# Optimization experiments

Hardware: AMD Instinct MI355X
Metric: run time of the kernel (lower is better)

The kernel has to match this reference:

```python
import jax, jax.numpy as jnp
import numpy as np

HEAD_NUM = 16
NEG_BIG = 1e12


def setup_inputs() -> dict:
    key = jax.random.key(0)
    ks = jax.random.split(key, 10)
    B, S, H = 4, 2048, 1024
    std = 0.02
    return {
        "encoder_outputs": jax.random.normal(ks[0], (B, S, H), dtype=jnp.float32),
        "mask": jax.random.randint(ks[1], (B, S), 0, 2, dtype=jnp.int32),
        "Wq": jax.random.normal(ks[2], (H, H), dtype=jnp.float32) * std,
        "bq": jax.random.normal(ks[3], (H,), dtype=jnp.float32) * std,
        "Wk": jax.random.normal(ks[4], (H, H), dtype=jnp.float32) * std,
        "bk": jax.random.normal(ks[5], (H,), dtype=jnp.float32) * std,
        "Wv": jax.random.normal(ks[6], (H, H), dtype=jnp.float32) * std,
        "bv": jax.random.normal(ks[7], (H,), dtype=jnp.float32) * std,
        "Wc": jax.random.normal(ks[8], (H, H), dtype=jnp.float32) * std,
    }


def _split_heads(x, h):
    # chunk(h, -1) + stack(dim=0): [B,S,H] -> [h,B,S,H//h]
    B, S, H = x.shape
    return jnp.moveaxis(x.reshape(B, S, h, H // h), 2, 0)


def reference(encoder_outputs, mask, Wq, bq, Wk, bk, Wv, bv, Wc):
    x = encoder_outputs
    B, S, H = x.shape
    hd = H // HEAD_NUM
    q = _split_heads(x @ Wq.T + bq, HEAD_NUM)  # [h,B,S,hd]
    k = _split_heads(x @ Wk.T + bk, HEAD_NUM)
    v = _split_heads(x @ Wv.T + bv, HEAD_NUM)
    dots = jnp.einsum("hbqd,hbkd->hbqk", q, k) / jnp.sqrt(jnp.float32(hd))
    m = mask.astype(jnp.float32)  # [B,S]; 0 = valid token
    inv = 1.0 - m
    eye = jnp.eye(S, dtype=jnp.float32)
    # clamp_max(1 - (1-m)_i (1-m)_j + eye, 1): [B,S,S]
    new_mask = jnp.minimum(1.0 - inv[:, :, None] * inv[:, None, :] + eye, 1.0)
    energies = dots - new_mask[None] * NEG_BIG
    weights = jax.nn.softmax(energies, axis=-1) * (1.0 - new_mask)[None]
    out = jnp.einsum("hbqk,hbkd->hbqd", weights, v)  # [h,B,S,hd]
    out = jnp.moveaxis(out, 0, 2).reshape(B, S, H)  # concat heads
    return out @ Wc.T
```

## Files before the change

### kernel.cpp

```cpp
#include <hip/hip_runtime.h>
#include <cstddef>
#include <cstdint>

#define BB 4
#define SS 2048
#define HH 1024
#define NH 16
#define HD 64

typedef _Float16 half8 __attribute__((ext_vector_type(8)));
typedef _Float16 half4v __attribute__((ext_vector_type(4)));
typedef float f32x4 __attribute__((ext_vector_type(4)));

#define KSCALE 0.1803368801111f

__device__ __forceinline__ void gload_lds16(const _Float16* g, char* l) {
    __builtin_amdgcn_global_load_lds(
        (const __attribute__((address_space(1))) void*)g,
        (__attribute__((address_space(3))) void*)l, 16, 0, 0);
}

__global__ __launch_bounds__(256)
void scan_mask(const int* __restrict__ mk, int* __restrict__ vidx,
               int* __restrict__ ividx, int* __restrict__ cnt)
{
    __shared__ int ps[256];
    const int b = blockIdx.x, t = threadIdx.x;
    int flag[8], s = 0;
#pragma unroll
    for (int k = 0; k < 8; ++k) { flag[k] = (mk[(b << 11) + t * 8 + k] == 0); s += flag[k]; }
    ps[t] = s;
    __syncthreads();
    for (int off = 1; off < 256; off <<= 1) {
        const int add = (t >= off) ? ps[t - off] : 0;
        __syncthreads();
        ps[t] += add;
        __syncthreads();
    }
    int posv = ps[t] - s;
#pragma unroll
    for (int k = 0; k < 8; ++k) {
        const int gidx = t * 8 + k;
        if (flag[k]) vidx[(b << 11) + posv++] = gidx;
        else         ividx[(b << 11) + (gidx - posv)] = gidx;
    }
    if (t == 255) cnt[b] = ps[255];
}

__global__ __launch_bounds__(256)
void prep_rows(const float* __restrict__ x, const int* __restrict__ vidx,
               const int* __restrict__ ividx, const int* __restrict__ cnt,
               _Float16* __restrict__ xc, float* __restrict__ out)
{
    const int row = blockIdx.x;
    const int b = row >> 11, i = row & 2047;
    const int t = threadIdx.x;
    const int cb = cnt[b];
    half4v hv = (half4v){0, 0, 0, 0};
    if (i < cb) {
        const float4 v = ((const float4*)(x + (size_t)((b << 11) + vidx[row]) * HH))[t];
        hv[0] = (_Float16)v.x; hv[1] = (_Float16)v.y;
        hv[2] = (_Float16)v.z; hv[3] = (_Float16)v.w;
    }
    ((half4v*)(xc + (size_t)row * HH))[t] = hv;
    if (i < SS - cb) {
        float* p = out + (size_t)((b << 11) + ividx[row]) * HH;
        ((float4*)p)[t] = make_float4(0.f, 0.f, 0.f, 0.f);
    }
}

__global__ __launch_bounds__(256)
void cvt_w(const float* __restrict__ Wq, const float* __restrict__ Wk,
           const float* __restrict__ Wv, const float* __restrict__ Wc,
           _Float16* __restrict__ o)
{
    const float* src = blockIdx.z == 0 ? Wq : blockIdx.z == 1 ? Wk :
                       blockIdx.z == 2 ? Wv : Wc;
    _Float16* dst = o + (size_t)blockIdx.z * (HH * HH);
    const int i = blockIdx.x * 256 + threadIdx.x;
    const float4 v0 = ((const float4*)src)[(size_t)i * 2];
    const float4 v1 = ((const float4*)src)[(size_t)i * 2 + 1];
    half8 hv;
    hv[0] = (_Float16)v0.x; hv[1] = (_Float16)v0.y;
    hv[2] = (_Float16)v0.z; hv[3] = (_Float16)v0.w;
    hv[4] = (_Float16)v1.x; hv[5] = (_Float16)v1.y;
    hv[6] = (_Float16)v1.z; hv[7] = (_Float16)v1.w;
    ((half8*)dst)[i] = hv;
}

__device__ __forceinline__ void gemm_core128(const _Float16* __restrict__ A,
                                             const _Float16* __restrict__ W,
                                             int K, int m0, int n0,
                                             char* As, char* Bs, f32x4 acc[4][4])
{
    const int t = threadIdx.x;
    const int w = t >> 6, lane = t & 63;
    const int ln = lane & 15, g = lane >> 4;
    const int wr = w >> 1, wc = w & 1;

    const int rr0 = w * 16 + (lane >> 2);
    const int rr1 = rr0 + 64;
    const int p   = lane & 3;
    const int sl0 = p ^ ((rr0 >> 1) & 3);
    const int sl1 = p ^ ((rr1 >> 1) & 3);
    const _Float16* ga0 = A + (size_t)(m0 + rr0) * K + sl0 * 8;
    const _Float16* ga1 = A + (size_t)(m0 + rr1) * K + sl1 * 8;
    const _Float16* gb0 = W + (size_t)(n0 + rr0) * K + sl0 * 8;
    const _Float16* gb1 = W + (size_t)(n0 + rr1) * K + sl1 * 8;
    char* dA = As + w * 1024 + lane * 16;
    char* dB = Bs + w * 1024 + lane * 16;

    int offA[4], offB[4];
#pragma unroll
    for (int i = 0; i < 4; ++i) {
        const int ra = wr * 64 + i * 16 + ln;
        offA[i] = ra * 64 + ((g ^ ((ra >> 1) & 3)) << 4);
        const int rb = wc * 64 + i * 16 + ln;
        offB[i] = rb * 64 + ((g ^ ((rb >> 1) & 3)) << 4);
    }

#pragma unroll
    for (int i = 0; i < 4; ++i)
#pragma unroll
        for (int j = 0; j < 4; ++j) acc[i][j] = (f32x4){0.f, 0.f, 0.f, 0.f};

    gload_lds16(ga0, dA);
    gload_lds16(ga1, dA + 4096);
    gload_lds16(gb0, dB);
    gload_lds16(gb1, dB + 4096);
    gload_lds16(ga0 + 32, dA + 8192);
    gload_lds16(ga1 + 32, dA + 8192 + 4096);
    gload_lds16(gb0 + 32, dB + 8192);
    gload_lds16(gb1 + 32, dB + 8192 + 4096);

    const int ns = K / 32;
    for (int k = 0; k < ns; ++k) {
        if (k < ns - 1) { asm volatile("s_waitcnt vmcnt(4)" ::: "memory"); }
        else            { asm volatile("s_waitcnt vmcnt(0)" ::: "memory"); }
        __builtin_amdgcn_s_barrier();
        __builtin_amdgcn_sched_barrier(0);

        const char* Ab = As + ((k & 1) << 13);
        const char* Bb = Bs + ((k & 1) << 13);
        half8 af[4], bf[4];
#pragma unroll
        for (int i = 0; i < 4; ++i) af[i] = *(const half8*)(Ab + offA[i]);
#pragma unroll
        for (int j = 0; j < 4; ++j) bf[j] = *(const half8*)(Bb + offB[j]);

        asm volatile("s_waitcnt lgkmcnt(0)" ::: "memory");
        __builtin_amdgcn_s_barrier();
        __builtin_amdgcn_sched_barrier(0);

        if (k + 2 < ns) {
            const int nb = (k & 1) << 13;
            const int ko = (k + 2) * 32;
            gload_lds16(ga0 + ko, dA + nb);
            gload_lds16(ga1 + ko, dA + nb + 4096);
            gload_lds16(gb0 + ko, dB + nb);
            gload_lds16(gb1 + ko, dB + nb + 4096);
        }
#pragma unroll
        for (int i = 0; i < 4; ++i)
#pragma unroll
            for (int j = 0; j < 4; ++j)
                acc[i][j] = __builtin_amdgcn_mfma_f32_16x16x32_f16(af[i], bf[j], acc[i][j], 0, 0, 0);
    }
}

__global__ __launch_bounds__(512, 2)
void gemm_qkv(const _Float16* __restrict__ xc, const _Float16* __restrict__ W16,
              const float* __restrict__ bq, const float* __restrict__ bk,
              const float* __restrict__ bv, const int* __restrict__ cnt,
              _Float16* __restrict__ Qh, _Float16* __restrict__ Kh,
              _Float16* __restrict__ Vt)
{
    const int yb = blockIdx.y;
    const int bI = yb & 3;
    const int mt = yb >> 2;
    if (mt * 256 >= ((cnt[bI] + 255) & ~255)) return;
    const int m0 = (bI << 11) + mt * 256;

    __shared__ __align__(16) char As[32768];
    __shared__ __align__(16) char Bs[32768];
    const int n0 = blockIdx.x * 256;
    const int z = n0 >> 10;
    const float* bias = (z == 0) ? bq : (z == 1) ? bk : bv;

    const int t = threadIdx.x;
    const int w = t >> 6, lane = t & 63;
    const int ln = lane & 15, g = lane >> 4;
    const int wr = w >> 2, wc = w & 3;

    const int rr0 = t >> 2;
    const int rr1 = rr0 + 128;
    const int p   = t & 3;
    const int sl0 = p ^ ((rr0 >> 1) & 3);
    const int sl1 = p ^ ((rr1 >> 1) & 3);
    const _Float16* ga0 = xc  + (size_t)(m0 + rr0) * HH + sl0 * 8;
    const _Float16* ga1 = xc  + (size_t)(m0 + rr1) * HH + sl1 * 8;
    const _Float16* gb0 = W16 + (size_t)(n0 + rr0) * HH + sl0 * 8;
    const _Float16* gb1 = W16 + (size_t)(n0 + rr1) * HH + sl1 * 8;
    char* dA = As + t * 16;
    char* dB = Bs + t * 16;

    int offA[8], offB[4];
#pragma unroll
    for (int i = 0; i < 8; ++i) {
        const int ra = wr * 128 + i * 16 + ln;
        offA[i] = ra * 64 + ((g ^ ((ra >> 1) & 3)) << 4);
    }
#pragma unroll
    for (int j = 0; j < 4; ++j) {
        const int rb = wc * 64 + j * 16 + ln;
        offB[j] = rb * 64 + ((g ^ ((rb >> 1) & 3)) << 4);
    }

    f32x4 acc[8][4];
#pragma unroll
    for (int i = 0; i < 8; ++i)
#pragma unroll
        for (int j = 0; j < 4; ++j) acc[i][j] = (f32x4){0.f, 0.f, 0.f, 0.f};

    gload_lds16(ga0, dA);
    gload_lds16(ga1, dA + 8192);
    gload_lds16(gb0, dB);
    gload_lds16(gb1, dB + 8192);
    gload_lds16(ga0 + 32, dA + 16384);
    gload_lds16(ga1 + 32, dA + 16384 + 8192);
    gload_lds16(gb0 + 32, dB + 16384);
    gload_lds16(gb1 + 32, dB + 16384 + 8192);

    const int ns = HH / 32;
    for (int k = 0; k < ns; ++k) {
        if (k < ns - 1) { asm volatile("s_waitcnt vmcnt(4)" ::: "memory"); }
        else            { asm volatile("s_waitcnt vmcnt(0)" ::: "memory"); }
        __builtin_amdgcn_s_barrier();
        __builtin_amdgcn_sched_barrier(0);

        const char* Ab = As + ((k & 1) << 14);
        const char* Bb = Bs + ((k & 1) << 14);
        half8 af[8], bf[4];
#pragma unroll
        for (int i = 0; i < 8; ++i) af[i] = *(const half8*)(Ab + offA[i]);
#pragma unroll
        for (int j = 0; j < 4; ++j) bf[j] = *(const half8*)(Bb + offB[j]);

        asm volatile("s_waitcnt lgkmcnt(0)" ::: "memory");
        __builtin_amdgcn_s_barrier();
        __builtin_amdgcn_sched_barrier(0);

        if (k + 2 < ns) {
            const int nb = (k & 1) << 14;
            const int ko = (k + 2) * 32;
            gload_lds16(ga0 + ko, dA + nb);
            gload_lds16(ga1 + ko, dA + nb + 8192);
            gload_lds16(gb0 + ko, dB + nb);
            gload_lds16(gb1 + ko, dB + nb + 8192);
        }
#pragma unroll
        for (int i = 0; i < 8; ++i)
#pragma unroll
            for (int j = 0; j < 4; ++j)
                acc[i][j] = __builtin_amdgcn_mfma_f32_16x16x32_f16(af[i], bf[j], acc[i][j], 0, 0, 0);
    }

    const int mBase = m0 + wr * 128 + g * 4;
    const int nBase = n0 + wc * 64 + ln;
    if (z < 2) {
        _Float16* O = z ? Kh : Qh;
        const float sc = z ? 1.0f : KSCALE;
#pragma unroll
        for (int j = 0; j < 4; ++j) {
            const int nn = (nBase + j * 16) & 1023;
            const int h = nn >> 6, d = nn & 63;
            const float bvf = bias[nn];
#pragma unroll
            for (int i = 0; i < 8; ++i) {
                const int m = mBase + i * 16;
                const int b = m >> 11, s = m & 2047;
                _Float16* dst = O + (((size_t)(b * NH + h) * SS + s) * HD + d);
#pragma unroll
                for (int r = 0; r < 4; ++r)
                    dst[(size_t)r * HD] = (_Float16)((acc[i][j][r] + bvf) * sc);
            }
        }
    } else {
#pragma unroll
        for (int j = 0; j < 4; ++j) {
            const int nn = (nBase + j * 16) & 1023;
            const int h = nn >> 6, d = nn & 63;
            const float bvf = bias[nn];
#pragma unroll
            for (int i = 0; i < 8; ++i) {
                const int m = mBase + i * 16;
                const int b = m >> 11, s = m & 2047;
                const int sp = (s & ~31) | (((s >> 2) & 3) << 3) | (((s >> 4) & 1) << 2);
                half4v v;
#pragma unroll
                for (int r = 0; r < 4; ++r) v[r] = (_Float16)(acc[i][j][r] + bvf);
                *(half4v*)(Vt + ((size_t)(b * NH + h) * HD + d) * SS + sp) = v;
            }
        }
    }
}

__global__ __launch_bounds__(256)
void gemm_out(const _Float16* __restrict__ Oc, const _Float16* __restrict__ Wc16,
              const int* __restrict__ cnt, const int* __restrict__ vidx,
              float* __restrict__ C)
{
    const int yb = blockIdx.y;
    const int bI = yb & 3;
    const int mt = yb >> 2;
    const int cb = cnt[bI];
    if (mt * 128 >= ((cb + 127) & ~127)) return;
    const int m0 = (bI << 11) + mt * 128;

    __shared__ __align__(16) char As[16384];
    __shared__ __align__(16) char Bs[16384];
    const int n0 = blockIdx.x * 128;

    f32x4 acc[4][4];
    gemm_core128(Oc, Wc16, HH, m0, n0, As, Bs, acc);

    const int t = threadIdx.x;
    const int w = t >> 6, lane = t & 63;
    const int ln = lane & 15, g = lane >> 4;
    const int wr = w >> 1, wc = w & 1;
    const int mBase = m0 + wr * 64 + g * 4;
    const int nBase = n0 + wc * 64 + ln;
#pragma unroll
    for (int i = 0; i < 4; ++i) {
#pragma unroll
        for (int r = 0; r < 4; ++r) {
            const int m = mBase + i * 16 + r;
            const int lm = m & 2047;
            if (lm < cb) {
                const int orig = vidx[m];
                const size_t off = (size_t)((m & ~2047) + orig) * HH + nBase;
#pragma unroll
                for (int j = 0; j < 4; ++j)
                    C[off + j * 16] = acc[i][j][r];
            }
        }
    }
}

__global__ __launch_bounds__(512, 4)
void attn_mfma(const _Float16* __restrict__ Qh, const _Float16* __restrict__ Kh,
               const _Float16* __restrict__ Vt, const int* __restrict__ cnt,
               _Float16* __restrict__ Oc)
{
    __shared__ __align__(16) char ksm[3][8192];
    __shared__ __align__(16) char vsm[3][8192];

    const int t  = threadIdx.x;
    const int w  = t >> 6, l = t & 63, ln = l & 15, g = l >> 4;
    const int bh = blockIdx.x;
    const int b  = bh >> 4, h = bh & 15;
    const int cb = cnt[b];
    const int q0 = blockIdx.y << 6;
    if (q0 >= cb) return;
    const int p  = w & 3;
    const int hf = w >> 2;
    const int qw = q0 + (p << 4);
    const bool active = (qw < cb);
    const int nt = (cb + 63) >> 6;
    const int jtd = qw >> 6;
    const int rel = (qw & 63) + ln;

    half8 qf[2];
    f32x4 oacc[4];
    float lrun = 0.f;
    if (active) {
        const int qg = qw + ln;
        const _Float16* qp = Qh + ((size_t)bh * SS + qg) * HD + g * 8;
        qf[0] = *(const half8*)qp;
        qf[1] = *(const half8*)(qp + 32);
#pragma unroll
        for (int dd = 0; dd < 4; ++dd) oacc[dd] = (f32x4){0.f, 0.f, 0.f, 0.f};
    }

    const int sr = t >> 3;
    const int sl = (t & 7) ^ (sr & 7);
    const _Float16* kbase = Kh + ((size_t)bh * SS + sr) * HD + sl * 8;
    const _Float16* vbase = Vt + ((size_t)bh * HD + sr) * SS + sl * 8;

    gload_lds16(kbase, ksm[0] + t * 16);
    gload_lds16(vbase, vsm[0] + t * 16);
    if (nt > 1) {
        gload_lds16(kbase + (size_t)64 * HD, ksm[1] + t * 16);
        gload_lds16(vbase + 64,              vsm[1] + t * 16);
    }

    int cur = 0;
    for (int jt = 0; jt < nt; ++jt) {
        if (jt < nt - 1) { asm volatile("s_waitcnt vmcnt(2) lgkmcnt(0)" ::: "memory"); }
        else             { asm volatile("s_waitcnt vmcnt(0) lgkmcnt(0)" ::: "memory"); }
        __builtin_amdgcn_s_barrier();
        __builtin_amdgcn_sched_barrier(0);

        if (jt + 2 < nt) {
            const int nb = (cur + 2 >= 3) ? cur - 1 : cur + 2;
            const int jn = (jt + 2) << 6;
            gload_lds16(kbase + (size_t)jn * HD, ksm[nb] + t * 16);
            gload_lds16(vbase + jn,              vsm[nb] + t * 16);
        }

        if (active) {
            const int j0 = jt << 6;
            const char* kb = ksm[cur];
            const char* vb = vsm[cur];
            half8 kf[2][2];
#pragma unroll
            for (int tu = 0; tu < 2; ++tu) {
                const int row = (hf * 2 + tu) * 16 + ln;
                const int sw  = (row & 7) << 4;
                const int rb  = row * 128;
                kf[tu][0] = *(const half8*)(kb + ((rb + g * 16)      ^ sw));
                kf[tu][1] = *(const half8*)(kb + ((rb + 64 + g * 16) ^ sw));
            }
            const bool slow = (jt == jtd) | (j0 + 64 > cb);

            f32x4 sa[2];
            __builtin_amdgcn_s_setprio(1);
#pragma unroll
            for (int tu = 0; tu < 2; ++tu) {
                sa[tu] = (f32x4){0.f, 0.f, 0.f, 0.f};
                sa[tu] = __builtin_amdgcn_mfma_f32_16x16x32_f16(kf[tu][0], qf[0], sa[tu], 0, 0, 0);
                sa[tu] = __builtin_amdgcn_mfma_f32_16x16x32_f16(kf[tu][1], qf[1], sa[tu], 0, 0, 0);
            }
            __builtin_amdgcn_s_setprio(0);

            float wv[2][4];
#pragma unroll
            for (int tu = 0; tu < 2; ++tu)
#pragma unroll
                for (int r = 0; r < 4; ++r) {
                    float tv = sa[tu][r];
                    if (slow) {
                        const int kp = (hf * 2 + tu) * 16 + g * 4 + r;
                        if (((jt == jtd) & (kp == rel)) | (j0 + kp >= cb))
                            tv = -1e30f;
                    }
                    wv[tu][r] = exp2f(tv);
                }
            lrun += ((wv[0][0] + wv[0][1]) + (wv[0][2] + wv[0][3]))
                  + ((wv[1][0] + wv[1][1]) + (wv[1][2] + wv[1][3]));

            half8 pf;
            pf[0] = (_Float16)wv[0][0]; pf[1] = (_Float16)wv[0][1];
            pf[2] = (_Float16)wv[0][2]; pf[3] = (_Float16)wv[0][3];
            pf[4] = (_Float16)wv[1][0]; pf[5] = (_Float16)wv[1][1];
            pf[6] = (_Float16)wv[1][2]; pf[7] = (_Float16)wv[1][3];

            __builtin_amdgcn_s_setprio(1);
#pragma unroll
            for (int dd = 0; dd < 4; ++dd) {
                const int row = dd * 16 + ln;
                const int sw  = (row & 7) << 4;
                const int rb  = row * 128;
                const half8 vf = *(const half8*)(vb + ((rb + hf * 64 + g * 16) ^ sw));
                oacc[dd] = __builtin_amdgcn_mfma_f32_16x16x32_f16(vf, pf, oacc[dd], 0, 0, 0);
            }
            __builtin_amdgcn_s_setprio(0);
        }
        cur = (cur + 1 == 3) ? 0 : cur + 1;
    }

    __syncthreads();
    f32x4* cmo = (f32x4*)vsm;
    float* cml = (float*)(cmo + 1024);
    if (active && hf == 1) {
#pragma unroll
        for (int dd = 0; dd < 4; ++dd) cmo[(p * 4 + dd) * 64 + l] = oacc[dd];
        cml[p * 64 + l] = lrun;
    }
    __syncthreads();
    if (active && hf == 0) {
#pragma unroll
        for (int dd = 0; dd < 4; ++dd) oacc[dd] += cmo[(p * 4 + dd) * 64 + l];
        float ls = lrun + cml[p * 64 + l];
        ls += __shfl_xor(ls, 16);
        ls += __shfl_xor(ls, 32);
        const int iq = qw + ln;
        if (iq < cb) {
            const float inv = (ls > 0.f) ? 1.f / ls : 0.f;
            _Float16* op = Oc + ((size_t)((b << 11) + iq)) * HH + h * HD + g * 4;
#pragma unroll
            for (int dd = 0; dd < 4; ++dd) {
                half4v hv;
#pragma unroll
                for (int r = 0; r < 4; ++r) hv[r] = (_Float16)(oacc[dd][r] * inv);
                *(half4v*)(op + dd * 16) = hv;
            }
        }
    }
}

extern "C" void kernel_launch(void* const* d_in, const int* in_sizes, int n_in,
                              void* d_out, int out_size, void* d_ws, size_t ws_size,
                              hipStream_t stream)
{
    (void)in_sizes; (void)n_in; (void)out_size; (void)ws_size;

    const float* x  = (const float*)d_in[0];
    const int*   mk = (const int*)d_in[1];
    const float* Wq = (const float*)d_in[2];
    const float* bq = (const float*)d_in[3];
    const float* Wk = (const float*)d_in[4];
    const float* bk = (const float*)d_in[5];
    const float* Wv = (const float*)d_in[6];
    const float* bv = (const float*)d_in[7];
    const float* Wc = (const float*)d_in[8];
    float* out = (float*)d_out;

    const int M = BB * SS;
    const size_t NE = (size_t)M * HH;
    const size_t NW = (size_t)HH * HH;
    _Float16* xc  = (_Float16*)d_ws;
    _Float16* W16 = xc + NE;
    _Float16* Qh  = W16 + 4 * NW;
    _Float16* Kh  = Qh + NE;
    _Float16* Vt  = Kh + NE;
    _Float16* Oc  = Vt + NE;
    int* vidx  = (int*)(Oc + NE);
    int* cnt   = vidx + M;
    int* ividx = cnt + 64;

    scan_mask<<<BB, 256, 0, stream>>>(mk, vidx, ividx, cnt);
    prep_rows<<<M, 256, 0, stream>>>(x, vidx, ividx, cnt, xc, out);
    cvt_w<<<dim3(512, 1, 4), 256, 0, stream>>>(Wq, Wk, Wv, Wc, W16);

    dim3 gq(3 * HH / 256, M / 256);
    gemm_qkv<<<gq, 512, 0, stream>>>(xc, W16, bq, bk, bv, cnt, Qh, Kh, Vt);

    dim3 ga(BB * NH, SS / 64);
    attn_mfma<<<ga, 512, 0, stream>>>(Qh, Kh, Vt, cnt, Oc);

    dim3 go(HH / 128, M / 128);
    gemm_out<<<go, 256, 0, stream>>>(Oc, W16 + 3 * NW, cnt, vidx, out);
}
```

Measured before the change: 122.9 us.

## Process two query sub-tiles per wave in attention to reuse K/V fragments

Each attention block now covers 128 query rows instead of 64. Each wave handles two 16-row query slices, so every K and V fragment read from LDS feeds two MFMAs, and each K/V tile loaded into shared memory serves twice as many queries. This halves the number of blocks and the total K/V traffic into shared memory. The cost is more registers (launch bounds lowered from 4 to 2 blocks per CU), fewer blocks to spread across the CUs, and a cross-wave combine step that now loops twice with extra barriers.

```diff
diff --git a/kernel.cpp b/kernel.cpp
--- a/kernel.cpp
+++ b/kernel.cpp
@@ -347,7 +347,7 @@
     }
 }
 
-__global__ __launch_bounds__(512, 4)
+__global__ __launch_bounds__(512, 2)
 void attn_mfma(const _Float16* __restrict__ Qh, const _Float16* __restrict__ Kh,
                const _Float16* __restrict__ Vt, const int* __restrict__ cnt,
                _Float16* __restrict__ Oc)
@@ -360,26 +360,30 @@
     const int bh = blockIdx.x;
     const int b  = bh >> 4, h = bh & 15;
     const int cb = cnt[b];
-    const int q0 = blockIdx.y << 6;
+    const int q0 = blockIdx.y << 7;
     if (q0 >= cb) return;
     const int p  = w & 3;
     const int hf = w >> 2;
-    const int qw = q0 + (p << 4);
+    const int qw = q0 + (p << 5);
     const bool active = (qw < cb);
     const int nt = (cb + 63) >> 6;
     const int jtd = qw >> 6;
-    const int rel = (qw & 63) + ln;
-
-    half8 qf[2];
-    f32x4 oacc[4];
-    float lrun = 0.f;
+    const int relb = (qw & 63) + ln;
+
+    half8 qf[2][2];
+    f32x4 oacc[2][4];
+    float lrun[2];
     if (active) {
-        const int qg = qw + ln;
-        const _Float16* qp = Qh + ((size_t)bh * SS + qg) * HD + g * 8;
-        qf[0] = *(const half8*)qp;
-        qf[1] = *(const half8*)(qp + 32);
-#pragma unroll
-        for (int dd = 0; dd < 4; ++dd) oacc[dd] = (f32x4){0.f, 0.f, 0.f, 0.f};
+#pragma unroll
+        for (int qs = 0; qs < 2; ++qs) {
+            const int qg = qw + qs * 16 + ln;
+            const _Float16* qp = Qh + ((size_t)bh * SS + qg) * HD + g * 8;
+            qf[qs][0] = *(const half8*)qp;
+            qf[qs][1] = *(const half8*)(qp + 32);
+            lrun[qs] = 0.f;
+#pragma unroll
+            for (int dd = 0; dd < 4; ++dd) oacc[qs][dd] = (f32x4){0.f, 0.f, 0.f, 0.f};
+        }
     }
 
     const int sr = t >> 3;
@@ -423,37 +427,44 @@
             }
             const bool slow = (jt == jtd) | (j0 + 64 > cb);
 
-            f32x4 sa[2];
+            f32x4 sa[2][2];
             __builtin_amdgcn_s_setprio(1);
 #pragma unroll
             for (int tu = 0; tu < 2; ++tu) {
-                sa[tu] = (f32x4){0.f, 0.f, 0.f, 0.f};
-                sa[tu] = __builtin_amdgcn_mfma_f32_16x16x32_f16(kf[tu][0], qf[0], sa[tu], 0, 0, 0);
-                sa[tu] = __builtin_amdgcn_mfma_f32_16x16x32_f16(kf[tu][1], qf[1], sa[tu], 0, 0, 0);
+#pragma unroll
+                for (int qs = 0; qs < 2; ++qs) {
+                    sa[qs][tu] = (f32x4){0.f, 0.f, 0.f, 0.f};
+                    sa[qs][tu] = __builtin_amdgcn_mfma_f32_16x16x32_f16(kf[tu][0], qf[qs][0], sa[qs][tu], 0, 0, 0);
+                    sa[qs][tu] = __builtin_amdgcn_mfma_f32_16x16x32_f16(kf[tu][1], qf[qs][1], sa[qs][tu], 0, 0, 0);
+                }
             }
             __builtin_amdgcn_s_setprio(0);
 
-            float wv[2][4];
-#pragma unroll
-            for (int tu = 0; tu < 2; ++tu)
-#pragma unroll
-                for (int r = 0; r < 4; ++r) {
-                    float tv = sa[tu][r];
-                    if (slow) {
-                        const int kp = (hf * 2 + tu) * 16 + g * 4 + r;
-                        if (((jt == jtd) & (kp == rel)) | (j0 + kp >= cb))
-                            tv = -1e30f;
+            half8 pf[2];
+#pragma unroll
+            for (int qs = 0; qs < 2; ++qs) {
+                float wv[2][4];
+#pragma unroll
+                for (int tu = 0; tu < 2; ++tu)
+#pragma unroll
+                    for (int r = 0; r < 4; ++r) {
+                        float tv = sa[qs][tu][r];
+                        if (slow) {
+                            const int kp = (hf * 2 + tu) * 16 + g * 4 + r;
+                            if (((jt == jtd) & (kp == relb + qs * 16)) | (j0 + kp >= cb))
+                                tv = -1e30f;
+                        }
+                        wv[tu][r] = exp2f(tv);
                     }
-                    wv[tu][r] = exp2f(tv);
-                }
-            lrun += ((wv[0][0] + wv[0][1]) + (wv[0][2] + wv[0][3]))
-                  + ((wv[1][0] + wv[1][1]) + (wv[1][2] + wv[1][3]));
-
-            half8 pf;
-            pf[0] = (_Float16)wv[0][0]; pf[1] = (_Float16)wv[0][1];
-            pf[2] = (_Float16)wv[0][2]; pf[3] = (_Float16)wv[0][3];
-            pf[4] = (_Float16)wv[1][0]; pf[5] = (_Float16)wv[1][1];
-            pf[6] = (_Float16)wv[1][2]; pf[7] = (_Float16)wv[1][3];
+                lrun[qs] += ((wv[0][0] + wv[0][1]) + (wv[0][2] + wv[0][3]))
+                          + ((wv[1][0] + wv[1][1]) + (wv[1][2] + wv[1][3]));
+                half8 pp;
+                pp[0] = (_Float16)wv[0][0]; pp[1] = (_Float16)wv[0][1];
+                pp[2] = (_Float16)wv[0][2]; pp[3] = (_Float16)wv[0][3];
+                pp[4] = (_Float16)wv[1][0]; pp[5] = (_Float16)wv[1][1];
+                pp[6] = (_Float16)wv[1][2]; pp[7] = (_Float16)wv[1][3];
+                pf[qs] = pp;
+            }
 
             __builtin_amdgcn_s_setprio(1);
 #pragma unroll
@@ -462,38 +473,44 @@
                 const int sw  = (row & 7) << 4;
                 const int rb  = row * 128;
                 const half8 vf = *(const half8*)(vb + ((rb + hf * 64 + g * 16) ^ sw));
-                oacc[dd] = __builtin_amdgcn_mfma_f32_16x16x32_f16(vf, pf, oacc[dd], 0, 0, 0);
+#pragma unroll
+                for (int qs = 0; qs < 2; ++qs)
+                    oacc[qs][dd] = __builtin_amdgcn_mfma_f32_16x16x32_f16(vf, pf[qs], oacc[qs][dd], 0, 0, 0);
             }
             __builtin_amdgcn_s_setprio(0);
         }
         cur = (cur + 1 == 3) ? 0 : cur + 1;
     }
 
-    __syncthreads();
-    f32x4* cmo = (f32x4*)vsm;
-    float* cml = (float*)(cmo + 1024);
-    if (active && hf == 1) {
-#pragma unroll
-        for (int dd = 0; dd < 4; ++dd) cmo[(p * 4 + dd) * 64 + l] = oacc[dd];
-        cml[p * 64 + l] = lrun;
-    }
-    __syncthreads();
-    if (active && hf == 0) {
-#pragma unroll
-        for (int dd = 0; dd < 4; ++dd) oacc[dd] += cmo[(p * 4 + dd) * 64 + l];
-        float ls = lrun + cml[p * 64 + l];
-        ls += __shfl_xor(ls, 16);
-        ls += __shfl_xor(ls, 32);
-        const int iq = qw + ln;
-        if (iq < cb) {
-            const float inv = (ls > 0.f) ? 1.f / ls : 0.f;
-            _Float16* op = Oc + ((size_t)((b << 11) + iq)) * HH + h * HD + g * 4;
-#pragma unroll
-            for (int dd = 0; dd < 4; ++dd) {
-                half4v hv;
-#pragma unroll
-                for (int r = 0; r < 4; ++r) hv[r] = (_Float16)(oacc[dd][r] * inv);
-                *(half4v*)(op + dd * 16) = hv;
+    f32x4* cmo = (f32x4*)ksm;
+    float*  cml = (float*)vsm;
+#pragma unroll
+    for (int qs = 0; qs < 2; ++qs) {
+        __syncthreads();
+        if (active && hf == 1) {
+#pragma unroll
+            for (int dd = 0; dd < 4; ++dd) cmo[(p * 4 + dd) * 64 + l] = oacc[qs][dd];
+            cml[p * 64 + l] = lrun[qs];
+        }
+        __syncthreads();
+        if (active && hf == 0) {
+            f32x4 o[4];
+#pragma unroll
+            for (int dd = 0; dd < 4; ++dd) o[dd] = oacc[qs][dd] + cmo[(p * 4 + dd) * 64 + l];
+            float ls = lrun[qs] + cml[p * 64 + l];
+            ls += __shfl_xor(ls, 16);
+            ls += __shfl_xor(ls, 32);
+            const int iq = qw + qs * 16 + ln;
+            if (iq < cb) {
+                const float inv = (ls > 0.f) ? 1.f / ls : 0.f;
+                _Float16* op = Oc + ((size_t)((b << 11) + iq)) * HH + h * HD + g * 4;
+#pragma unroll
+                for (int dd = 0; dd < 4; ++dd) {
+                    half4v hv;
+#pragma unroll
+                    for (int r = 0; r < 4; ++r) hv[r] = (_Float16)(o[dd][r] * inv);
+                    *(half4v*)(op + dd * 16) = hv;
+                }
             }
         }
     }
@@ -536,7 +553,7 @@
     dim3 gq(3 * HH / 256, M / 256);
     gemm_qkv<<<gq, 512, 0, stream>>>(xc, W16, bq, bk, bv, cnt, Qh, Kh, Vt);
 
-    dim3 ga(BB * NH, SS / 64);
+    dim3 ga(BB * NH, SS / 128);
     attn_mfma<<<ga, 512, 0, stream>>>(Qh, Kh, Vt, cnt, Oc);
 
     dim3 go(HH / 128, M / 128);
```

Result: slower. 134.0 us (+9.1%).

## Merge weight conversion into prep kernel and double-buffer attention K/V

Applied to the files above, without the earlier changes.

Folds the fp32-to-fp16 weight conversion into the row-prep kernel as extra blocks, removing one kernel launch and letting both run concurrently. In the attention kernel, the three-stage K/V LDS ring becomes a two-stage double buffer, cutting shared memory from 48KB to 32KB, which may allow more resident blocks. The cost is less prefetch depth: each iteration now waits for every outstanding load before computing. The combine scratch is moved to fit within the smaller buffers.

```diff
diff --git a/kernel.cpp b/kernel.cpp
--- a/kernel.cpp
+++ b/kernel.cpp
@@ -50,11 +50,30 @@
 __global__ __launch_bounds__(256)
 void prep_rows(const float* __restrict__ x, const int* __restrict__ vidx,
                const int* __restrict__ ividx, const int* __restrict__ cnt,
-               _Float16* __restrict__ xc, float* __restrict__ out)
-{
-    const int row = blockIdx.x;
+               _Float16* __restrict__ xc, float* __restrict__ out,
+               const float* __restrict__ Wq, const float* __restrict__ Wk,
+               const float* __restrict__ Wv, const float* __restrict__ Wc,
+               _Float16* __restrict__ W16)
+{
+    const int t = threadIdx.x;
+    const int blk = blockIdx.x;
+    if (blk >= BB * SS) {
+        const int wi = (blk - BB * SS) * 256 + t;
+        const int z = wi >> 17, idx = wi & 131071;
+        const float* src = z == 0 ? Wq : z == 1 ? Wk : z == 2 ? Wv : Wc;
+        _Float16* dst = W16 + (size_t)z * (HH * HH);
+        const float4 v0 = ((const float4*)src)[(size_t)idx * 2];
+        const float4 v1 = ((const float4*)src)[(size_t)idx * 2 + 1];
+        half8 hv;
+        hv[0] = (_Float16)v0.x; hv[1] = (_Float16)v0.y;
+        hv[2] = (_Float16)v0.z; hv[3] = (_Float16)v0.w;
+        hv[4] = (_Float16)v1.x; hv[5] = (_Float16)v1.y;
+        hv[6] = (_Float16)v1.z; hv[7] = (_Float16)v1.w;
+        ((half8*)dst)[idx] = hv;
+        return;
+    }
+    const int row = blk;
     const int b = row >> 11, i = row & 2047;
-    const int t = threadIdx.x;
     const int cb = cnt[b];
     half4v hv = (half4v){0, 0, 0, 0};
     if (i < cb) {
@@ -67,25 +86,6 @@
         float* p = out + (size_t)((b << 11) + ividx[row]) * HH;
         ((float4*)p)[t] = make_float4(0.f, 0.f, 0.f, 0.f);
     }
-}
-
-__global__ __launch_bounds__(256)
-void cvt_w(const float* __restrict__ Wq, const float* __restrict__ Wk,
-           const float* __restrict__ Wv, const float* __restrict__ Wc,
-           _Float16* __restrict__ o)
-{
-    const float* src = blockIdx.z == 0 ? Wq : blockIdx.z == 1 ? Wk :
-                       blockIdx.z == 2 ? Wv : Wc;
-    _Float16* dst = o + (size_t)blockIdx.z * (HH * HH);
-    const int i = blockIdx.x * 256 + threadIdx.x;
-    const float4 v0 = ((const float4*)src)[(size_t)i * 2];
-    const float4 v1 = ((const float4*)src)[(size_t)i * 2 + 1];
-    half8 hv;
-    hv[0] = (_Float16)v0.x; hv[1] = (_Float16)v0.y;
-    hv[2] = (_Float16)v0.z; hv[3] = (_Float16)v0.w;
-    hv[4] = (_Float16)v1.x; hv[5] = (_Float16)v1.y;
-    hv[6] = (_Float16)v1.z; hv[7] = (_Float16)v1.w;
-    ((half8*)dst)[i] = hv;
 }
 
 __device__ __forceinline__ void gemm_core128(const _Float16* __restrict__ A,
@@ -352,8 +352,8 @@
                const _Float16* __restrict__ Vt, const int* __restrict__ cnt,
                _Float16* __restrict__ Oc)
 {
-    __shared__ __align__(16) char ksm[3][8192];
-    __shared__ __align__(16) char vsm[3][8192];
+    __shared__ __align__(16) char ksm[2][8192];
+    __shared__ __align__(16) char vsm[2][8192];
 
     const int t  = threadIdx.x;
     const int w  = t >> 6, l = t & 63, ln = l & 15, g = l >> 4;
@@ -389,23 +389,17 @@
 
     gload_lds16(kbase, ksm[0] + t * 16);
     gload_lds16(vbase, vsm[0] + t * 16);
-    if (nt > 1) {
-        gload_lds16(kbase + (size_t)64 * HD, ksm[1] + t * 16);
-        gload_lds16(vbase + 64,              vsm[1] + t * 16);
-    }
 
     int cur = 0;
     for (int jt = 0; jt < nt; ++jt) {
-        if (jt < nt - 1) { asm volatile("s_waitcnt vmcnt(2) lgkmcnt(0)" ::: "memory"); }
-        else             { asm volatile("s_waitcnt vmcnt(0) lgkmcnt(0)" ::: "memory"); }
+        asm volatile("s_waitcnt vmcnt(0) lgkmcnt(0)" ::: "memory");
         __builtin_amdgcn_s_barrier();
         __builtin_amdgcn_sched_barrier(0);
 
-        if (jt + 2 < nt) {
-            const int nb = (cur + 2 >= 3) ? cur - 1 : cur + 2;
-            const int jn = (jt + 2) << 6;
-            gload_lds16(kbase + (size_t)jn * HD, ksm[nb] + t * 16);
-            gload_lds16(vbase + jn,              vsm[nb] + t * 16);
+        if (jt + 1 < nt) {
+            const int jn = (jt + 1) << 6;
+            gload_lds16(kbase + (size_t)jn * HD, ksm[cur ^ 1] + t * 16);
+            gload_lds16(vbase + jn,              vsm[cur ^ 1] + t * 16);
         }
 
         if (active) {
@@ -466,12 +460,12 @@
             }
             __builtin_amdgcn_s_setprio(0);
         }
-        cur = (cur + 1 == 3) ? 0 : cur + 1;
+        cur ^= 1;
     }
 
     __syncthreads();
-    f32x4* cmo = (f32x4*)vsm;
-    float* cml = (float*)(cmo + 1024);
+    f32x4* cmo = (f32x4*)ksm;
+    float*  cml = (float*)vsm;
     if (active && hf == 1) {
 #pragma unroll
         for (int dd = 0; dd < 4; ++dd) cmo[(p * 4 + dd) * 64 + l] = oacc[dd];
@@ -530,8 +524,8 @@
     int* ividx = cnt + 64;
 
     scan_mask<<<BB, 256, 0, stream>>>(mk, vidx, ividx, cnt);
-    prep_rows<<<M, 256, 0, stream>>>(x, vidx, ividx, cnt, xc, out);
-    cvt_w<<<dim3(512, 1, 4), 256, 0, stream>>>(Wq, Wk, Wv, Wc, W16);
+    prep_rows<<<M + 2048, 256, 0, stream>>>(x, vidx, ividx, cnt, xc, out,
+                                            Wq, Wk, Wv, Wc, W16);
 
     dim3 gq(3 * HH / 256, M / 256);
     gemm_qkv<<<gq, 512, 0, stream>>>(xc, W16, bq, bk, bv, cnt, Qh, Kh, Vt);
```

New measurement: 121.0 us, median of 3. Within noise of the previous version (-1.5%).
